# Kernel tuning notes

Measured on AMD Instinct MI355X. Metric: run time of the kernel, lower is better.

The kernel has to match this reference:

```python
import jax, jax.numpy as jnp
import numpy as np

D_MODEL = 1024
D_FF = 4096
N_EXPERTS = 8
TOP_K = 2

def setup_inputs() -> dict:
    key = jax.random.key(0)
    ks = jax.random.split(key, 8)
    s = 1.0 / np.sqrt(D_MODEL)
    sf = 1.0 / np.sqrt(D_FF)
    return {
        "x": jax.random.normal(ks[0], (4, 1024, D_MODEL), dtype=jnp.float32),
        "W1": jax.random.uniform(ks[1], (N_EXPERTS, D_MODEL, D_FF), jnp.float32, -s, s),
        "b1": jax.random.uniform(ks[2], (N_EXPERTS, D_FF), jnp.float32, -s, s),
        "W2": jax.random.uniform(ks[3], (N_EXPERTS, D_FF, D_MODEL), jnp.float32, -sf, sf),
        "b2": jax.random.uniform(ks[4], (N_EXPERTS, D_MODEL), jnp.float32, -sf, sf),
        "Wg": jax.random.uniform(ks[5], (D_MODEL, N_EXPERTS), jnp.float32, -s, s),
        "bg": jax.random.uniform(ks[6], (N_EXPERTS,), jnp.float32, -s, s),
    }

def reference(x, W1, b1, W2, b2, Wg, bg):
    # gate: [B,S,E]
    logits = jnp.einsum('bsd,de->bse', x, Wg) + bg
    probs = jax.nn.softmax(logits, axis=-1)
    # top-k mask + renormalize (k < n_experts)
    topk_vals, topk_idx = jax.lax.top_k(probs, TOP_K)
    mask = jax.nn.one_hot(topk_idx, N_EXPERTS, dtype=probs.dtype).sum(axis=-2)
    probs = probs * mask
    denom = probs.sum(axis=-1, keepdims=True)
    denom = denom + (denom == 0).astype(probs.dtype)
    probs = probs / denom
    # dense expert compute: all experts on all tokens. h: [B,E,S,d_ff]
    h = jnp.einsum('bsd,edf->besf', x, W1) + b1[None, :, None, :]
    h = jax.nn.gelu(h, approximate=False)
    y = jnp.einsum('besf,efd->besd', h, W2) + b2[None, :, None, :]
    # weighted combine over experts: [B,S,d]
    out = jnp.einsum('bse,besd->bsd', probs, y)
    return out
```

## Files before the change

kernel.cpp:

```cpp
#include <hip/hip_runtime.h>
#include <hip/hip_bf16.h>

#define NTOK   4096
#define DMODEL 1024
#define DFF    4096
#define NEXP   8
#define TOPK   2
#define BM 128
#define BN 128
#define BK 64
#define NSLOT   (NTOK*TOPK)
#define MAXSLOT (NSLOT + NEXP*BM)
#define MAXTILE (MAXSLOT/BM)
#define NWTILE  8192

typedef __attribute__((ext_vector_type(8))) short bf16x8;
typedef __attribute__((ext_vector_type(8))) unsigned short u16x8;
typedef __attribute__((ext_vector_type(4))) float f32x4;

__device__ __forceinline__ unsigned short f2bf(float f){
    union { float f; unsigned int u; } v; v.f = f;
    unsigned int r = (v.u + 0x7fffu + ((v.u >> 16) & 1u)) >> 16;
    return (unsigned short)r;
}

__device__ __forceinline__ void gload16(const unsigned short* g, unsigned short* l){
    __builtin_amdgcn_global_load_lds(
        (const __attribute__((address_space(1))) void*)g,
        (__attribute__((address_space(3))) void*)l,
        16, 0, 0);
}

__device__ __forceinline__ void transpose_tile64(const float* __restrict__ src,
                                                 unsigned short* __restrict__ dst,
                                                 int R, int C, int r0, int c0,
                                                 float (*tile)[65])
{
    int t = threadIdx.x;
    int tr  = t >> 4;
    int tc4 = (t & 15) * 4;
    #pragma unroll
    for(int i=0;i<4;i++){
        float4 v = *(const float4*)&src[(size_t)(r0 + tr + i*16)*C + c0 + tc4];
        tile[tc4+0][tr + i*16] = v.x;
        tile[tc4+1][tr + i*16] = v.y;
        tile[tc4+2][tr + i*16] = v.z;
        tile[tc4+3][tr + i*16] = v.w;
    }
    __syncthreads();
    int cr = t >> 3;
    int rb = (t & 7) * 8;
    #pragma unroll
    for(int i=0;i<2;i++){
        int c = cr + i*32;
        u16x8 o;
        #pragma unroll
        for(int q=0;q<8;q++) o[q] = f2bf(tile[c][rb + q]);
        *(u16x8*)&dst[(size_t)(c0 + c)*R + r0 + rb] = o;
    }
    __syncthreads();
}

__global__ __launch_bounds__(256) void k_gate_w1t(const float* __restrict__ x,
                                                  const float* __restrict__ Wg,
                                                  const float* __restrict__ bg,
                                                  const float* __restrict__ W1,
                                                  unsigned short* __restrict__ Xb,
                                                  unsigned short* __restrict__ W1t,
                                                  float* __restrict__ out,
                                                  int* __restrict__ token_e,
                                                  float* __restrict__ token_w,
                                                  int* __restrict__ cnt)
{
    __shared__ float tile[64][65];
    int bx = blockIdx.x;
    if(bx % 3 != 0){
        int w = bx - bx/3 - 1;
        for(int t2 = w; t2 < NWTILE; t2 += 2048){
            int z  = t2 >> 10;
            int rem = t2 & 1023;
            int rt = rem >> 6;
            int ct = rem & 63;
            transpose_tile64(W1 + (size_t)z*DMODEL*DFF, W1t + (size_t)z*DMODEL*DFF,
                             DMODEL, DFF, rt*64, ct*64, tile);
        }
        return;
    }
    int b = bx / 3;
    int tid = threadIdx.x;
    const float4* xs = (const float4*)x + (size_t)b * 1024;
    ushort4* xd = (ushort4*)Xb + (size_t)b * 1024;
    float4* oz = (float4*)out + (size_t)b * 1024;
    float4 z4 = {0.f,0.f,0.f,0.f};
    #pragma unroll
    for(int rep=0;rep<4;rep++){
        float4 v = xs[rep*256 + tid];
        ushort4 o; o.x=f2bf(v.x); o.y=f2bf(v.y); o.z=f2bf(v.z); o.w=f2bf(v.w);
        xd[rep*256 + tid] = o;
        oz[rep*256 + tid] = z4;
    }

    int wid = tid >> 6, lane = tid & 63;
    int t = b * 4 + wid;
    const float* xr = x + (size_t)t * DMODEL;
    float pe[NEXP];
    #pragma unroll
    for(int e=0;e<NEXP;e++) pe[e] = 0.f;
    for(int i=0;i<DMODEL/64;i++){
        int d = i*64 + lane;
        float xv = xr[d];
        const float* wr = Wg + (size_t)d * NEXP;
        #pragma unroll
        for(int e=0;e<NEXP;e++) pe[e] += xv * wr[e];
    }
    #pragma unroll
    for(int off=32; off>0; off>>=1){
        #pragma unroll
        for(int e=0;e<NEXP;e++) pe[e] += __shfl_xor(pe[e], off);
    }
    if(lane == 0){
        float lg[NEXP], mx = -1e30f;
        #pragma unroll
        for(int e=0;e<NEXP;e++){ lg[e] = pe[e] + bg[e]; mx = fmaxf(mx, lg[e]); }
        float pr[NEXP];
        #pragma unroll
        for(int e=0;e<NEXP;e++) pr[e] = expf(lg[e] - mx);
        int e0 = 0; float p0 = pr[0];
        #pragma unroll
        for(int e=1;e<NEXP;e++) if(pr[e] > p0){ p0 = pr[e]; e0 = e; }
        int e1 = -1; float p1 = -1.f;
        #pragma unroll
        for(int e=0;e<NEXP;e++) if(e != e0 && pr[e] > p1){ p1 = pr[e]; e1 = e; }
        float dn = p0 + p1;
        token_e[2*t]   = e0; token_w[2*t]   = p0/dn;
        token_e[2*t+1] = e1; token_w[2*t+1] = p1/dn;
        atomicAdd(&cnt[e0], 1); atomicAdd(&cnt[e1], 1);
    }
}

__global__ __launch_bounds__(256) void k_prefix(const int* __restrict__ cnt,
                                                int* __restrict__ tile_e,
                                                int* __restrict__ tile_row0,
                                                int* __restrict__ tile_valid,
                                                int* __restrict__ cursor,
                                                int* __restrict__ slot_token)
{
    int tid = threadIdx.x;
    if(tid == 0){
        int off = 0, nt = 0;
        for(int e=0;e<NEXP;e++){
            cursor[e] = off;
            int c = cnt[e];
            for(int r=0;r<c;r+=BM){
                tile_e[nt] = e; tile_row0[nt] = off + r;
                tile_valid[nt] = (c - r < BM) ? (c - r) : BM;
                nt++;
            }
            off += ((c + BM - 1)/BM)*BM;
        }
        for(int i=nt;i<MAXTILE;i++){ tile_e[i]=0; tile_row0[i]=0; tile_valid[i]=0; }
    }
    for(int s=tid; s<MAXSLOT; s+=256) slot_token[s] = 0;
}

__global__ __launch_bounds__(256) void k_scatter(const int* __restrict__ token_e,
                                                 const float* __restrict__ token_w,
                                                 int* __restrict__ cursor,
                                                 int* __restrict__ slot_token,
                                                 float* __restrict__ slot_w)
{
    int i = blockIdx.x*256 + threadIdx.x;
    int e = token_e[i];
    int s = atomicAdd(&cursor[e], 1);
    slot_token[s] = i >> 1;
    slot_w[s] = token_w[i];
}

template<bool GATHER, bool GELU, bool FUSET>
__global__ __launch_bounds__(256, 3) void k_gemm(const unsigned short* __restrict__ A,
                                                 const unsigned short* __restrict__ Bw,
                                                 const float* __restrict__ bias,
                                                 const int* __restrict__ tile_e,
                                                 const int* __restrict__ tile_row0,
                                                 const int* __restrict__ tile_valid,
                                                 const int* __restrict__ slot_token,
                                                 const float* __restrict__ slot_w,
                                                 unsigned short* __restrict__ OutH,
                                                 float* __restrict__ outF,
                                                 const float* __restrict__ Wsrc,
                                                 unsigned short* __restrict__ Wdst,
                                                 int K, int N)
{
    __shared__ __align__(16) unsigned short SM[BM*BK + BN*BK];
    unsigned short* As = SM;
    unsigned short* Bs = SM + BM*BK;

    int y = blockIdx.y;
    if(FUSET && ((y+1) % 5) == 0){
        float (*tile)[65] = (float(*)[65])SM;
        int w = blockIdx.x * 8 + (y/5);
        for(int t2 = w; t2 < NWTILE; t2 += 576){
            int z  = t2 >> 10;
            int rem = t2 & 1023;
            int rt = rem >> 4;
            int ct = rem & 15;
            transpose_tile64(Wsrc + (size_t)z*DFF*DMODEL, Wdst + (size_t)z*DFF*DMODEL,
                             DFF, DMODEL, rt*64, ct*64, tile);
        }
        return;
    }

    int xb = blockIdx.x;
    int tid = (xb & 7) * (MAXTILE/8) + (xb >> 3);
    int valid = tile_valid[tid];
    if(valid == 0) return;
    int e = tile_e[tid];
    int row0 = tile_row0[tid];
    int n0 = (FUSET ? (y - (y+1)/5) : y) * BN;
    const unsigned short* Be = Bw + (size_t)e * N * K;

    int t = threadIdx.x;
    int lane = t & 63;
    int wid = t >> 6;
    int wr = wid >> 1, wc = wid & 1;

    int srow = t >> 3;
    int csw  = (t & 7) ^ (srow & 7);
    const unsigned short* arow[4];
    const unsigned short* brow[4];
    #pragma unroll
    for(int i=0;i<4;i++){
        int r = i*32 + srow;
        size_t aoff;
        if(GATHER) aoff = (size_t)slot_token[row0 + r] * (size_t)K;
        else       aoff = (size_t)(row0 + r) * (size_t)K;
        arow[i] = A  + aoff + csw*8;
        brow[i] = Be + (size_t)(n0 + r)*K + csw*8;
    }
    unsigned short* alds = As + (size_t)t * 8;
    unsigned short* blds = Bs + (size_t)t * 8;

    f32x4 acc[4][4];
    #pragma unroll
    for(int m=0;m<4;m++)
        #pragma unroll
        for(int n=0;n<4;n++)
            acc[m][n] = (f32x4){0.f,0.f,0.f,0.f};

    int rl = lane & 15;
    int g  = lane >> 4;
    int rx = rl & 7;

    for(int k0=0;k0<K;k0+=BK){
        __syncthreads();
        #pragma unroll
        for(int i=0;i<4;i++){
            gload16(arow[i] + k0, alds + i*2048);
            gload16(brow[i] + k0, blds + i*2048);
        }
        __syncthreads();

        #pragma unroll
        for(int kb=0;kb<2;kb++){
            int sw = ((kb*4 + g) ^ rx) * 8;
            bf16x8 af[4], bfv[4];
            #pragma unroll
            for(int m=0;m<4;m++) af[m]  = *(const bf16x8*)&As[(wr*64 + m*16 + rl)*BK + sw];
            #pragma unroll
            for(int n=0;n<4;n++) bfv[n] = *(const bf16x8*)&Bs[(wc*64 + n*16 + rl)*BK + sw];
            #pragma unroll
            for(int m=0;m<4;m++)
                #pragma unroll
                for(int n=0;n<4;n++)
                    acc[m][n] = __builtin_amdgcn_mfma_f32_16x16x32_bf16(af[m], bfv[n], acc[m][n], 0, 0, 0);
        }
    }

    const float* be = bias + (size_t)e * N;
    #pragma unroll
    for(int m=0;m<4;m++){
        int rb = wr*64 + m*16 + g*4;
        #pragma unroll
        for(int j=0;j<4;j++){
            int r = rb + j;
            if(r >= valid) continue;
            size_t grow = (size_t)(row0 + r);
            if(GELU){
                #pragma unroll
                for(int n=0;n<4;n++){
                    int col = n0 + wc*64 + n*16 + rl;
                    float v = acc[m][n][j] + be[col];
                    v = 0.5f * v * (1.f + erff(v * 0.70710678118654752f));
                    OutH[grow * (size_t)N + col] = f2bf(v);
                }
            } else {
                float wsc = slot_w[grow];
                float* orow = outF + (size_t)slot_token[grow] * DMODEL;
                #pragma unroll
                for(int n=0;n<4;n++){
                    int col = n0 + wc*64 + n*16 + rl;
                    float v = (acc[m][n][j] + be[col]) * wsc;
                    atomicAdd(&orow[col], v);
                }
            }
        }
    }
}

extern "C" void kernel_launch(void* const* d_in, const int* in_sizes, int n_in,
                              void* d_out, int out_size, void* d_ws, size_t ws_size,
                              hipStream_t stream)
{
    const float* x  = (const float*)d_in[0];
    const float* W1 = (const float*)d_in[1];
    const float* b1 = (const float*)d_in[2];
    const float* W2 = (const float*)d_in[3];
    const float* b2 = (const float*)d_in[4];
    const float* Wg = (const float*)d_in[5];
    const float* bg = (const float*)d_in[6];
    float* out = (float*)d_out;

    char* p = (char*)d_ws;
    auto alloc = [&](size_t bytes)->char*{
        char* r = p; p += (bytes + 255) & ~(size_t)255; return r;
    };
    unsigned short* W1t = (unsigned short*)alloc((size_t)NEXP*DFF*DMODEL*2);
    unsigned short* W2t = (unsigned short*)alloc((size_t)NEXP*DMODEL*DFF*2);
    unsigned short* Xb  = (unsigned short*)alloc((size_t)NTOK*DMODEL*2);
    unsigned short* H   = (unsigned short*)alloc((size_t)MAXSLOT*DFF*2);
    int*   slot_token = (int*)alloc(MAXSLOT*4);
    float* slot_w     = (float*)alloc(MAXSLOT*4);
    int*   token_e    = (int*)alloc(NSLOT*4);
    float* token_w    = (float*)alloc(NSLOT*4);
    int*   cnt        = (int*)alloc(64);
    int*   cursor     = (int*)alloc(64);
    int*   tile_e     = (int*)alloc(MAXTILE*4);
    int*   tile_row0  = (int*)alloc(MAXTILE*4);
    int*   tile_valid = (int*)alloc(MAXTILE*4);
    (void)ws_size; (void)in_sizes; (void)n_in; (void)out_size;

    hipMemsetAsync(cnt, 0, 64, stream);
    k_gate_w1t<<<3072, 256, 0, stream>>>(x, Wg, bg, W1, Xb, W1t, out,
                                         token_e, token_w, cnt);
    k_prefix<<<1, 256, 0, stream>>>(cnt, tile_e, tile_row0, tile_valid, cursor, slot_token);
    k_scatter<<<NSLOT/256, 256, 0, stream>>>(token_e, token_w, cursor, slot_token, slot_w);
    k_gemm<true, true, true ><<<dim3(MAXTILE, 40), 256, 0, stream>>>(
        Xb, W1t, b1, tile_e, tile_row0, tile_valid, slot_token, slot_w, H, nullptr,
        W2, W2t, DMODEL, DFF);
    k_gemm<false,false,false><<<dim3(MAXTILE, DMODEL/BN), 256, 0, stream>>>(
        H,  W2t, b2, tile_e, tile_row0, tile_valid, slot_token, slot_w, nullptr, out,
        nullptr, nullptr, DFF, DMODEL);
}
```

Before: 429.0 us.

## Split-K the second expert GEMM and double-buffer the W1 transpose tiles

The second expert GEMM (H times W2) is split into two halves along K via blockIdx.z. Each half accumulates into the output with atomics, and only the first half adds the bias. This doubles the grid for the small-N GEMM to raise occupancy, at the cost of twice as many atomic adds to the output. The W1 transpose blocks also now use a two-buffer shared tile, so the next tile is loaded while the current one is converted and stored.

Result: slower. 450.9 us (+5.1%).

```diff
diff --git a/kernel.cpp b/kernel.cpp
--- a/kernel.cpp
+++ b/kernel.cpp
@@ -72,22 +72,49 @@
                                                   float* __restrict__ token_w,
                                                   int* __restrict__ cnt)
 {
-    __shared__ float tile[64][65];
+    __shared__ float tile[2][64][65];
     int bx = blockIdx.x;
+    int tid = threadIdx.x;
     if(bx % 3 != 0){
         int w = bx - bx/3 - 1;
-        for(int t2 = w; t2 < NWTILE; t2 += 2048){
-            int z  = t2 >> 10;
-            int rem = t2 & 1023;
-            int rt = rem >> 6;
-            int ct = rem & 63;
-            transpose_tile64(W1 + (size_t)z*DMODEL*DFF, W1t + (size_t)z*DMODEL*DFF,
-                             DMODEL, DFF, rt*64, ct*64, tile);
+        int tr  = tid >> 4, tc4 = (tid & 15) * 4;
+        int cr  = tid >> 3, rb  = (tid & 7) * 8;
+        auto load_t = [&](int t2, int buf){
+            int z = t2 >> 10, rem = t2 & 1023;
+            const float* src = W1 + (size_t)z*DMODEL*DFF;
+            int r0 = (rem >> 6)*64, c0 = (rem & 63)*64;
+            #pragma unroll
+            for(int i=0;i<4;i++){
+                float4 v = *(const float4*)&src[(size_t)(r0 + tr + i*16)*DFF + c0 + tc4];
+                tile[buf][tc4+0][tr + i*16] = v.x;
+                tile[buf][tc4+1][tr + i*16] = v.y;
+                tile[buf][tc4+2][tr + i*16] = v.z;
+                tile[buf][tc4+3][tr + i*16] = v.w;
+            }
+        };
+        auto store_t = [&](int t2, int buf){
+            int z = t2 >> 10, rem = t2 & 1023;
+            unsigned short* dst = W1t + (size_t)z*DMODEL*DFF;
+            int r0 = (rem >> 6)*64, c0 = (rem & 63)*64;
+            #pragma unroll
+            for(int i=0;i<2;i++){
+                int c = cr + i*32;
+                u16x8 o;
+                #pragma unroll
+                for(int q=0;q<8;q++) o[q] = f2bf(tile[buf][c][rb + q]);
+                *(u16x8*)&dst[(size_t)(c0 + c)*DMODEL + r0 + rb] = o;
+            }
+        };
+        load_t(w, 0);
+        #pragma unroll
+        for(int j=0;j<4;j++){
+            __syncthreads();
+            if(j+1 < 4) load_t(w + (j+1)*2048, (j+1)&1);
+            store_t(w + j*2048, j&1);
         }
         return;
     }
     int b = bx / 3;
-    int tid = threadIdx.x;
     const float4* xs = (const float4*)x + (size_t)b * 1024;
     ushort4* xd = (ushort4*)Xb + (size_t)b * 1024;
     float4* oz = (float4*)out + (size_t)b * 1024;
@@ -189,7 +216,7 @@
                                                  float* __restrict__ outF,
                                                  const float* __restrict__ Wsrc,
                                                  unsigned short* __restrict__ Wdst,
-                                                 int K, int N)
+                                                 int lda, int N, int klen)
 {
     __shared__ __align__(16) unsigned short SM[BM*BK + BN*BK];
     unsigned short* As = SM;
@@ -217,7 +244,8 @@
     int e = tile_e[tid];
     int row0 = tile_row0[tid];
     int n0 = (FUSET ? (y - (y+1)/5) : y) * BN;
-    const unsigned short* Be = Bw + (size_t)e * N * K;
+    int kbase = blockIdx.z * klen;
+    const unsigned short* Be = Bw + (size_t)e * N * lda;
 
     int t = threadIdx.x;
     int lane = t & 63;
@@ -232,10 +260,10 @@
     for(int i=0;i<4;i++){
         int r = i*32 + srow;
         size_t aoff;
-        if(GATHER) aoff = (size_t)slot_token[row0 + r] * (size_t)K;
-        else       aoff = (size_t)(row0 + r) * (size_t)K;
-        arow[i] = A  + aoff + csw*8;
-        brow[i] = Be + (size_t)(n0 + r)*K + csw*8;
+        if(GATHER) aoff = (size_t)slot_token[row0 + r] * (size_t)lda;
+        else       aoff = (size_t)(row0 + r) * (size_t)lda;
+        arow[i] = A  + aoff + kbase + csw*8;
+        brow[i] = Be + (size_t)(n0 + r)*lda + kbase + csw*8;
     }
     unsigned short* alds = As + (size_t)t * 8;
     unsigned short* blds = Bs + (size_t)t * 8;
@@ -251,7 +279,7 @@
     int g  = lane >> 4;
     int rx = rl & 7;
 
-    for(int k0=0;k0<K;k0+=BK){
+    for(int k0=0;k0<klen;k0+=BK){
         __syncthreads();
         #pragma unroll
         for(int i=0;i<4;i++){
@@ -299,7 +327,8 @@
                 #pragma unroll
                 for(int n=0;n<4;n++){
                     int col = n0 + wc*64 + n*16 + rl;
-                    float v = (acc[m][n][j] + be[col]) * wsc;
+                    float bterm = (kbase == 0) ? be[col] : 0.f;
+                    float v = (acc[m][n][j] + bterm) * wsc;
                     atomicAdd(&orow[col], v);
                 }
             }
@@ -344,10 +373,10 @@
                                          token_e, token_w, cnt);
     k_prefix<<<1, 256, 0, stream>>>(cnt, tile_e, tile_row0, tile_valid, cursor, slot_token);
     k_scatter<<<NSLOT/256, 256, 0, stream>>>(token_e, token_w, cursor, slot_token, slot_w);
-    k_gemm<true, true, true ><<<dim3(MAXTILE, 40), 256, 0, stream>>>(
+    k_gemm<true, true, true ><<<dim3(MAXTILE, 40, 1), 256, 0, stream>>>(
         Xb, W1t, b1, tile_e, tile_row0, tile_valid, slot_token, slot_w, H, nullptr,
-        W2, W2t, DMODEL, DFF);
-    k_gemm<false,false,false><<<dim3(MAXTILE, DMODEL/BN), 256, 0, stream>>>(
+        W2, W2t, DMODEL, DFF, DMODEL);
+    k_gemm<false,false,false><<<dim3(MAXTILE, DMODEL/BN, 2), 256, 0, stream>>>(
         H,  W2t, b2, tile_e, tile_row0, tile_valid, slot_token, slot_w, nullptr, out,
-        nullptr, nullptr, DFF, DMODEL);
-}
+        nullptr, nullptr, DFF, DMODEL, DFF/2);
+}
```

## Rewrite first expert GEMM as 256x256 double-buffered pipelined kernel

Applied to the files above, without the earlier changes.

The first grouped GEMM moves to a dedicated 512-thread kernel with 256x256 tiles, a 64 KB double-buffered LDS, manual vmcnt/lgkmcnt waits, sched barriers and setprio to overlap global-to-LDS loads with MFMA work. The W2 transpose is reassigned to a fixed set of blocks with a vectorised bf16 store path. Expert slots are padded to 256 rows with separate tile tables for the two GEMMs, and the second GEMM keeps the old 128x128 design. The larger tiles increase data reuse, but they lower occupancy to one block per CU and add more padding waste for each expert.

New measurement: 448.2 us. 4.5% more time.

```diff
diff --git a/kernel.cpp b/kernel.cpp
--- a/kernel.cpp
+++ b/kernel.cpp
@@ -6,12 +6,10 @@
 #define DFF    4096
 #define NEXP   8
 #define TOPK   2
-#define BM 128
-#define BN 128
-#define BK 64
 #define NSLOT   (NTOK*TOPK)
-#define MAXSLOT (NSLOT + NEXP*BM)
-#define MAXTILE (MAXSLOT/BM)
+#define MAXSLOT (NSLOT + NEXP*256)
+#define NT2     40
+#define NT1     72
 #define NWTILE  8192
 
 typedef __attribute__((ext_vector_type(8))) short bf16x8;
@@ -29,6 +27,16 @@
         (const __attribute__((address_space(1))) void*)g,
         (__attribute__((address_space(3))) void*)l,
         16, 0, 0);
+}
+
+#define WAITLGKM() asm volatile("s_waitcnt lgkmcnt(0)" ::: "memory")
+#define WAITVM4()  asm volatile("s_waitcnt vmcnt(4)" ::: "memory")
+#define WAITVM0()  asm volatile("s_waitcnt vmcnt(0)" ::: "memory")
+#define SCHEDPIN() __builtin_amdgcn_sched_barrier(0)
+#define MFMA16(a,b,c) __builtin_amdgcn_mfma_f32_16x16x32_bf16(a,b,c,0,0,0)
+
+__device__ __forceinline__ bf16x8 ldswz(const unsigned short* lds, int base, int r, int kcol){
+    return *(const bf16x8*)&lds[base + r*64 + (kcol ^ ((r & 7) << 3))];
 }
 
 __device__ __forceinline__ void transpose_tile64(const float* __restrict__ src,
@@ -139,26 +147,31 @@
 }
 
 __global__ __launch_bounds__(256) void k_prefix(const int* __restrict__ cnt,
-                                                int* __restrict__ tile_e,
-                                                int* __restrict__ tile_row0,
-                                                int* __restrict__ tile_valid,
+                                                int* __restrict__ t2e, int* __restrict__ t2r,
+                                                int* __restrict__ t2v,
+                                                int* __restrict__ t1e, int* __restrict__ t1r,
+                                                int* __restrict__ t1v,
                                                 int* __restrict__ cursor,
                                                 int* __restrict__ slot_token)
 {
     int tid = threadIdx.x;
     if(tid == 0){
-        int off = 0, nt = 0;
+        int off = 0, n2 = 0, n1 = 0;
         for(int e=0;e<NEXP;e++){
             cursor[e] = off;
             int c = cnt[e];
-            for(int r=0;r<c;r+=BM){
-                tile_e[nt] = e; tile_row0[nt] = off + r;
-                tile_valid[nt] = (c - r < BM) ? (c - r) : BM;
-                nt++;
-            }
-            off += ((c + BM - 1)/BM)*BM;
-        }
-        for(int i=nt;i<MAXTILE;i++){ tile_e[i]=0; tile_row0[i]=0; tile_valid[i]=0; }
+            for(int r=0;r<c;r+=256){
+                t2e[n2] = e; t2r[n2] = off + r;
+                t2v[n2] = (c - r < 256) ? (c - r) : 256; n2++;
+            }
+            for(int r=0;r<c;r+=128){
+                t1e[n1] = e; t1r[n1] = off + r;
+                t1v[n1] = (c - r < 128) ? (c - r) : 128; n1++;
+            }
+            off += ((c + 255)/256)*256;
+        }
+        for(int i=n2;i<NT2;i++){ t2e[i]=0; t2r[i]=0; t2v[i]=0; }
+        for(int i=n1;i<NT1;i++){ t1e[i]=0; t1r[i]=0; t1v[i]=0; }
     }
     for(int s=tid; s<MAXSLOT; s+=256) slot_token[s] = 0;
 }
@@ -176,48 +189,232 @@
     slot_w[s] = token_w[i];
 }
 
-template<bool GATHER, bool GELU, bool FUSET>
-__global__ __launch_bounds__(256, 3) void k_gemm(const unsigned short* __restrict__ A,
-                                                 const unsigned short* __restrict__ Bw,
-                                                 const float* __restrict__ bias,
-                                                 const int* __restrict__ tile_e,
-                                                 const int* __restrict__ tile_row0,
-                                                 const int* __restrict__ tile_valid,
-                                                 const int* __restrict__ slot_token,
-                                                 const float* __restrict__ slot_w,
-                                                 unsigned short* __restrict__ OutH,
-                                                 float* __restrict__ outF,
-                                                 const float* __restrict__ Wsrc,
-                                                 unsigned short* __restrict__ Wdst,
-                                                 int K, int N)
-{
-    __shared__ __align__(16) unsigned short SM[BM*BK + BN*BK];
-    unsigned short* As = SM;
-    unsigned short* Bs = SM + BM*BK;
-
+__global__ __launch_bounds__(512, 1) void k_gemm1(const unsigned short* __restrict__ A,
+                                                  const unsigned short* __restrict__ Bw,
+                                                  const float* __restrict__ bias,
+                                                  const int* __restrict__ t2e,
+                                                  const int* __restrict__ t2r,
+                                                  const int* __restrict__ t2v,
+                                                  const int* __restrict__ slot_token,
+                                                  unsigned short* __restrict__ OutH,
+                                                  const float* __restrict__ W2,
+                                                  unsigned short* __restrict__ W2t)
+{
+    __shared__ unsigned short lds[65536];
+
+    int t = threadIdx.x;
     int y = blockIdx.y;
-    if(FUSET && ((y+1) % 5) == 0){
-        float (*tile)[65] = (float(*)[65])SM;
-        int w = blockIdx.x * 8 + (y/5);
-        for(int t2 = w; t2 < NWTILE; t2 += 576){
-            int z  = t2 >> 10;
-            int rem = t2 & 1023;
-            int rt = rem >> 4;
-            int ct = rem & 15;
-            transpose_tile64(Wsrc + (size_t)z*DFF*DMODEL, Wdst + (size_t)z*DFF*DMODEL,
-                             DFF, DMODEL, rt*64, ct*64, tile);
+    if(y < 4){
+        if(blockIdx.x >= 32) return;
+        int half = t >> 8, tl = t & 255;
+        float* fl = (float*)lds;
+        float (*tile)[65] = (float(*)[65])(fl + half*64*65);
+        int stream = (blockIdx.x*4 + y)*2 + half;
+        int tr = tl >> 4, tc4 = (tl & 15)*4;
+        int cr = tl >> 3, rb = (tl & 7)*8;
+        for(int j=0;j<32;j++){
+            int t2 = stream + j*256;
+            int z = t2 >> 10, rem = t2 & 1023;
+            const float* src = W2 + (size_t)z*DFF*DMODEL;
+            unsigned short* dst = W2t + (size_t)z*DFF*DMODEL;
+            int r0 = (rem >> 4)*64, c0 = (rem & 15)*64;
+            #pragma unroll
+            for(int i=0;i<4;i++){
+                float4 v = *(const float4*)&src[(size_t)(r0 + tr + i*16)*DMODEL + c0 + tc4];
+                tile[tc4+0][tr+i*16]=v.x; tile[tc4+1][tr+i*16]=v.y;
+                tile[tc4+2][tr+i*16]=v.z; tile[tc4+3][tr+i*16]=v.w;
+            }
+            __syncthreads();
+            #pragma unroll
+            for(int i=0;i<2;i++){
+                int c = cr + i*32;
+                u16x8 o;
+                #pragma unroll
+                for(int q=0;q<8;q++) o[q] = f2bf(tile[c][rb+q]);
+                *(u16x8*)&dst[(size_t)(c0 + c)*DFF + r0 + rb] = o;
+            }
+            __syncthreads();
         }
         return;
     }
 
     int xb = blockIdx.x;
-    int tid = (xb & 7) * (MAXTILE/8) + (xb >> 3);
-    int valid = tile_valid[tid];
+    int tid = (xb & 7) * 5 + (xb >> 3);
+    int valid = t2v[tid];
     if(valid == 0) return;
-    int e = tile_e[tid];
-    int row0 = tile_row0[tid];
-    int n0 = (FUSET ? (y - (y+1)/5) : y) * BN;
+    int e = t2e[tid], row0 = t2r[tid];
+    int n0 = (y - 4) * 256;
+    const int K = DMODEL, N = DFF;
     const unsigned short* Be = Bw + (size_t)e * N * K;
+
+    int lane = t & 63, wid = t >> 6;
+    int wm = wid >> 2, wn = wid & 3;
+    int rl = lane & 15, g = lane >> 4;
+
+    int r8  = t >> 3;
+    int ccs = (t & 7) ^ (r8 & 7);
+    const unsigned short* asrc[2][2];
+    const unsigned short* bsrc[2][2];
+    #pragma unroll
+    for(int h=0;h<2;h++){
+        #pragma unroll
+        for(int l=0;l<2;l++){
+            int r = h*128 + l*64 + r8;
+            size_t ar = (size_t)slot_token[row0 + r] * (size_t)K;
+            asrc[h][l] = A  + ar + ccs*8;
+            bsrc[h][l] = Be + (size_t)(n0 + r)*K + ccs*8;
+        }
+    }
+    int ldst = t * 8;
+
+#define SA1(kt,h,l) gload16(asrc[h][l] + (kt)*64, &lds[(((kt)&1)<<15) + ((h)<<13) + ((l)<<12) + ldst])
+#define SB1(kt,h,l) gload16(bsrc[h][l] + (kt)*64, &lds[(((kt)&1)<<15) + 16384 + ((h)<<13) + ((l)<<12) + ldst])
+
+    SA1(0,0,0); SA1(0,0,1); SA1(0,1,0); SA1(0,1,1);
+    SB1(0,0,0); SB1(0,0,1); SB1(0,1,0); SB1(0,1,1);
+    SB1(1,0,0); SB1(1,0,1); SB1(1,1,0); SB1(1,1,1);
+
+    f32x4 acc[8][4];
+    #pragma unroll
+    for(int i=0;i<8;i++)
+        #pragma unroll
+        for(int j=0;j<4;j++) acc[i][j] = (f32x4){0.f,0.f,0.f,0.f};
+
+    WAITVM4();
+    __builtin_amdgcn_s_barrier();
+
+    const int NK = K >> 6;
+    bf16x8 af[4][2], bfv[4][2];
+
+    for(int k=0;k<NK;k++){
+        int bufo = (k & 1) << 15;
+        bool stA = (k+1 < NK);
+        bool stB = (k+2 < NK);
+
+        #pragma unroll
+        for(int m=0;m<4;m++){
+            af[m][0] = ldswz(lds, bufo, wm*128 + m*16 + rl, g*8);
+            af[m][1] = ldswz(lds, bufo, wm*128 + m*16 + rl, 32 + g*8);
+        }
+        #pragma unroll
+        for(int n=0;n<2;n++){
+            bfv[n][0] = ldswz(lds, bufo + 16384, wn*64 + n*16 + rl, g*8);
+            bfv[n][1] = ldswz(lds, bufo + 16384, wn*64 + n*16 + rl, 32 + g*8);
+        }
+        if(stA){ SA1(k+1,0,0); SA1(k+1,0,1); }
+        __builtin_amdgcn_s_barrier();
+        WAITLGKM();
+        SCHEDPIN();
+        __builtin_amdgcn_s_setprio(1);
+        #pragma unroll
+        for(int m=0;m<4;m++)
+            #pragma unroll
+            for(int n=0;n<2;n++){
+                acc[m][n] = MFMA16(af[m][0], bfv[n][0], acc[m][n]);
+                acc[m][n] = MFMA16(af[m][1], bfv[n][1], acc[m][n]);
+            }
+        __builtin_amdgcn_s_setprio(0);
+        __builtin_amdgcn_s_barrier();
+
+        #pragma unroll
+        for(int n=2;n<4;n++){
+            bfv[n][0] = ldswz(lds, bufo + 16384, wn*64 + n*16 + rl, g*8);
+            bfv[n][1] = ldswz(lds, bufo + 16384, wn*64 + n*16 + rl, 32 + g*8);
+        }
+        if(stA){ SA1(k+1,1,0); SA1(k+1,1,1); }
+        __builtin_amdgcn_s_barrier();
+        WAITLGKM();
+        SCHEDPIN();
+        __builtin_amdgcn_s_setprio(1);
+        #pragma unroll
+        for(int m=0;m<4;m++)
+            #pragma unroll
+            for(int n=2;n<4;n++){
+                acc[m][n] = MFMA16(af[m][0], bfv[n][0], acc[m][n]);
+                acc[m][n] = MFMA16(af[m][1], bfv[n][1], acc[m][n]);
+            }
+        __builtin_amdgcn_s_setprio(0);
+        __builtin_amdgcn_s_barrier();
+
+        #pragma unroll
+        for(int m=0;m<4;m++){
+            af[m][0] = ldswz(lds, bufo, wm*128 + 64 + m*16 + rl, g*8);
+            af[m][1] = ldswz(lds, bufo, wm*128 + 64 + m*16 + rl, 32 + g*8);
+        }
+        if(stB){ SB1(k+2,0,0); SB1(k+2,0,1); }
+        __builtin_amdgcn_s_barrier();
+        WAITLGKM();
+        SCHEDPIN();
+        __builtin_amdgcn_s_setprio(1);
+        #pragma unroll
+        for(int m=0;m<4;m++)
+            #pragma unroll
+            for(int n=0;n<2;n++){
+                acc[4+m][n] = MFMA16(af[m][0], bfv[n][0], acc[4+m][n]);
+                acc[4+m][n] = MFMA16(af[m][1], bfv[n][1], acc[4+m][n]);
+            }
+        __builtin_amdgcn_s_setprio(0);
+        __builtin_amdgcn_s_barrier();
+
+        if(stB){ SB1(k+2,1,0); SB1(k+2,1,1); }
+        __builtin_amdgcn_s_barrier();
+        __builtin_amdgcn_s_setprio(1);
+        #pragma unroll
+        for(int m=0;m<4;m++)
+            #pragma unroll
+            for(int n=2;n<4;n++){
+                acc[4+m][n] = MFMA16(af[m][0], bfv[n][0], acc[4+m][n]);
+                acc[4+m][n] = MFMA16(af[m][1], bfv[n][1], acc[4+m][n]);
+            }
+        __builtin_amdgcn_s_setprio(0);
+        if(stB)      { WAITVM4(); }
+        else if(stA) { WAITVM0(); }
+        __builtin_amdgcn_s_barrier();
+    }
+#undef SA1
+#undef SB1
+
+    const float* be = bias + (size_t)e * N;
+    #pragma unroll
+    for(int mi=0;mi<8;mi++){
+        int rbse = wm*128 + mi*16 + g*4;
+        #pragma unroll
+        for(int j=0;j<4;j++){
+            int r = rbse + j;
+            if(r >= valid) continue;
+            size_t grow = (size_t)(row0 + r);
+            #pragma unroll
+            for(int n=0;n<4;n++){
+                int col = n0 + wn*64 + n*16 + rl;
+                float v = acc[mi][n][j] + be[col];
+                v = 0.5f * v * (1.f + erff(v * 0.70710678118654752f));
+                OutH[grow * (size_t)N + col] = f2bf(v);
+            }
+        }
+    }
+}
+
+__global__ __launch_bounds__(256, 3) void k_gemm2(const unsigned short* __restrict__ A,
+                                                  const unsigned short* __restrict__ Bw,
+                                                  const float* __restrict__ bias,
+                                                  const int* __restrict__ t1e,
+                                                  const int* __restrict__ t1r,
+                                                  const int* __restrict__ t1v,
+                                                  const int* __restrict__ slot_token,
+                                                  const float* __restrict__ slot_w,
+                                                  float* __restrict__ outF)
+{
+    const int K = DFF, N = DMODEL;
+    int xb = blockIdx.x;
+    int tid = (xb & 7) * 9 + (xb >> 3);
+    int valid = t1v[tid];
+    if(valid == 0) return;
+    int e = t1e[tid], row0 = t1r[tid];
+    int n0 = blockIdx.y * 128;
+    const unsigned short* Be = Bw + (size_t)e * N * K;
+
+    __shared__ unsigned short As[128*64];
+    __shared__ unsigned short Bs[128*64];
 
     int t = threadIdx.x;
     int lane = t & 63;
@@ -231,10 +428,7 @@
     #pragma unroll
     for(int i=0;i<4;i++){
         int r = i*32 + srow;
-        size_t aoff;
-        if(GATHER) aoff = (size_t)slot_token[row0 + r] * (size_t)K;
-        else       aoff = (size_t)(row0 + r) * (size_t)K;
-        arow[i] = A  + aoff + csw*8;
+        arow[i] = A  + (size_t)(row0 + r) * (size_t)K + csw*8;
         brow[i] = Be + (size_t)(n0 + r)*K + csw*8;
     }
     unsigned short* alds = As + (size_t)t * 8;
@@ -251,7 +445,7 @@
     int g  = lane >> 4;
     int rx = rl & 7;
 
-    for(int k0=0;k0<K;k0+=BK){
+    for(int k0=0;k0<K;k0+=64){
         __syncthreads();
         #pragma unroll
         for(int i=0;i<4;i++){
@@ -265,14 +459,14 @@
             int sw = ((kb*4 + g) ^ rx) * 8;
             bf16x8 af[4], bfv[4];
             #pragma unroll
-            for(int m=0;m<4;m++) af[m]  = *(const bf16x8*)&As[(wr*64 + m*16 + rl)*BK + sw];
-            #pragma unroll
-            for(int n=0;n<4;n++) bfv[n] = *(const bf16x8*)&Bs[(wc*64 + n*16 + rl)*BK + sw];
+            for(int m=0;m<4;m++) af[m]  = *(const bf16x8*)&As[(wr*64 + m*16 + rl)*64 + sw];
+            #pragma unroll
+            for(int n=0;n<4;n++) bfv[n] = *(const bf16x8*)&Bs[(wc*64 + n*16 + rl)*64 + sw];
             #pragma unroll
             for(int m=0;m<4;m++)
                 #pragma unroll
                 for(int n=0;n<4;n++)
-                    acc[m][n] = __builtin_amdgcn_mfma_f32_16x16x32_bf16(af[m], bfv[n], acc[m][n], 0, 0, 0);
+                    acc[m][n] = MFMA16(af[m], bfv[n], acc[m][n]);
         }
     }
 
@@ -285,23 +479,13 @@
             int r = rb + j;
             if(r >= valid) continue;
             size_t grow = (size_t)(row0 + r);
-            if(GELU){
-                #pragma unroll
-                for(int n=0;n<4;n++){
-                    int col = n0 + wc*64 + n*16 + rl;
-                    float v = acc[m][n][j] + be[col];
-                    v = 0.5f * v * (1.f + erff(v * 0.70710678118654752f));
-                    OutH[grow * (size_t)N + col] = f2bf(v);
-                }
-            } else {
-                float wsc = slot_w[grow];
-                float* orow = outF + (size_t)slot_token[grow] * DMODEL;
-                #pragma unroll
-                for(int n=0;n<4;n++){
-                    int col = n0 + wc*64 + n*16 + rl;
-                    float v = (acc[m][n][j] + be[col]) * wsc;
-                    atomicAdd(&orow[col], v);
-                }
+            float wsc = slot_w[grow];
+            float* orow = outF + (size_t)slot_token[grow] * DMODEL;
+            #pragma unroll
+            for(int n=0;n<4;n++){
+                int col = n0 + wc*64 + n*16 + rl;
+                float v = (acc[m][n][j] + be[col]) * wsc;
+                atomicAdd(&orow[col], v);
             }
         }
     }
@@ -334,20 +518,21 @@
     float* token_w    = (float*)alloc(NSLOT*4);
     int*   cnt        = (int*)alloc(64);
     int*   cursor     = (int*)alloc(64);
-    int*   tile_e     = (int*)alloc(MAXTILE*4);
-    int*   tile_row0  = (int*)alloc(MAXTILE*4);
-    int*   tile_valid = (int*)alloc(MAXTILE*4);
+    int*   t2e = (int*)alloc(NT2*4);
+    int*   t2r = (int*)alloc(NT2*4);
+    int*   t2v = (int*)alloc(NT2*4);
+    int*   t1e = (int*)alloc(NT1*4);
+    int*   t1r = (int*)alloc(NT1*4);
+    int*   t1v = (int*)alloc(NT1*4);
     (void)ws_size; (void)in_sizes; (void)n_in; (void)out_size;
 
     hipMemsetAsync(cnt, 0, 64, stream);
     k_gate_w1t<<<3072, 256, 0, stream>>>(x, Wg, bg, W1, Xb, W1t, out,
                                          token_e, token_w, cnt);
-    k_prefix<<<1, 256, 0, stream>>>(cnt, tile_e, tile_row0, tile_valid, cursor, slot_token);
+    k_prefix<<<1, 256, 0, stream>>>(cnt, t2e, t2r, t2v, t1e, t1r, t1v, cursor, slot_token);
     k_scatter<<<NSLOT/256, 256, 0, stream>>>(token_e, token_w, cursor, slot_token, slot_w);
-    k_gemm<true, true, true ><<<dim3(MAXTILE, 40), 256, 0, stream>>>(
-        Xb, W1t, b1, tile_e, tile_row0, tile_valid, slot_token, slot_w, H, nullptr,
-        W2, W2t, DMODEL, DFF);
-    k_gemm<false,false,false><<<dim3(MAXTILE, DMODEL/BN), 256, 0, stream>>>(
-        H,  W2t, b2, tile_e, tile_row0, tile_valid, slot_token, slot_w, nullptr, out,
-        nullptr, nullptr, DFF, DMODEL);
-}
+    k_gemm1<<<dim3(NT2, 20), 512, 0, stream>>>(
+        Xb, W1t, b1, t2e, t2r, t2v, slot_token, H, W2, W2t);
+    k_gemm2<<<dim3(NT1, DMODEL/128), 256, 0, stream>>>(
+        H, W2t, b2, t1e, t1r, t1v, slot_token, slot_w, out);
+}
```
